# Performance work log

Hardware: AMD Instinct MI355X
Metric: run time of the kernel (lower is better)

## Reference

```python
import jax, jax.numpy as jnp
import numpy as np

CLASS_DIM = 4   # hardcoded in DsFunction1
PROTO_DIM = 20  # hardcoded in DsFunction1


def setup_inputs() -> dict:
    key = jax.random.key(0)
    k1, k2, k3 = jax.random.split(key, 3)
    B, C, H, Wd, D = 2, 16, 64, 64, 64
    inp = jax.random.normal(k1, (B, C, H, Wd, D), dtype=jnp.float32)
    W = jax.random.normal(k2, (PROTO_DIM, C), dtype=jnp.float32)
    BETA = jax.random.normal(k3, (PROTO_DIM, CLASS_DIM), dtype=jnp.float32) * 0.5
    alpha = jnp.zeros((PROTO_DIM, 1), dtype=jnp.float32)           # init 0 per reset_parameters
    gamma = jnp.full((PROTO_DIM, 1), 0.1, dtype=jnp.float32)       # init 0.1 per reset_parameters
    return {"input": inp, "W": W, "BETA": BETA, "alpha": alpha, "gamma": gamma}


def _ds_forward(x, W, BETA, alpha, gamma):
    # x: [B,C,H,Wd,D]; W: [K,C]; BETA: [K,M]; alpha, gamma: [K,1]
    B, C, H, Wd, D = x.shape
    BETA2 = BETA * BETA
    U = BETA2 / jnp.sum(BETA2, axis=1, keepdims=True)              # [K,M] membership weights
    alphap = 0.99 / (1.0 + jnp.exp(-alpha[:, 0]))                  # [K]

    # squared distances to prototypes: d[k] = 0.5 * ||x - W_k||^2 over channel dim
    x2 = jnp.sum(x * x, axis=1)                                    # [B,H,Wd,D]
    xw = jnp.einsum('bchwd,kc->kbhwd', x, W)                       # [K,B,H,Wd,D]
    w2 = jnp.sum(W * W, axis=1)                                    # [K]
    d = 0.5 * (x2[None] - 2.0 * xw + w2[:, None, None, None, None])  # [K,B,H,Wd,D]

    g2 = (gamma[:, 0] ** 2)[:, None, None, None, None]
    s = alphap[:, None, None, None, None] * jnp.exp(-g2 * d)       # [K,B,H,Wd,D]

    mfoc = U[:, :, None, None, None, None] * s[:, None]            # [K,M,B,H,Wd,D] focal masses
    momega = 1.0 - s                                               # [K,B,H,Wd,D] mass on Omega

    # sequential Dempster (unnormalized conjunctive) combination over prototypes
    def step(carry, km):
        mk_f, mk_o = carry                                         # [M,B,H,Wd,D], [B,H,Wd,D]
        m_f, m_o = km
        new_f = mk_f * (m_f + m_o[None]) + m_f * mk_o[None]
        new_o = mk_o * m_o
        return (new_f, new_o), None

    init = (jnp.zeros((CLASS_DIM, B, H, Wd, D), x.dtype),
            jnp.ones((B, H, Wd, D), x.dtype))
    (mk_f, mk_o), _ = jax.lax.scan(step, init, (mfoc, momega))

    mk = jnp.concatenate([mk_f, mk_o[None]], axis=0)               # [M+1,B,H,Wd,D]
    mk_n = mk / jnp.sum(mk, axis=0, keepdims=True)                 # normalize masses
    return jnp.transpose(mk_n, (1, 0, 2, 3, 4))                    # [B,M+1,H,Wd,D]


def reference(input, W, BETA, alpha, gamma):
    return _ds_forward(input, W, BETA, alpha, gamma)
```

## Files before the change

### kernel.cpp

```cpp
#include <hip/hip_runtime.h>
#include <hip/hip_bf16.h>
#include <math.h>

#define NK 20
#define NC 16
#define NM 4
#define TSTEP 2

typedef __attribute__((ext_vector_type(8)))  short  short8;
typedef __attribute__((ext_vector_type(16))) float  floatx16;

static __device__ __forceinline__ short bf16b(float f) {
    __hip_bfloat16 h = __float2bfloat16(f);
    return *reinterpret_cast<short*>(&h);
}

__global__ __launch_bounds__(256, 4) void ds_fused(
    const float* __restrict__ inp,
    const float* __restrict__ Wg,
    const float* __restrict__ BETAg,
    const float* __restrict__ alphag,
    const float* __restrict__ gammag,
    float* __restrict__ out,
    int S,
    int BS)
{
    __shared__ __align__(16) float sCst[32][8];
    __shared__ __align__(16) short sWpb[32][16];
    __shared__ short sA2[32][2];

    const int t = threadIdx.x;
    if (t < 32) {
        if (t < NK) {
            const float L   = 1.4426950408889634f;
            const float g   = gammag[t];
            const float g2L = g * g * L;
            float w2 = 0.f;
            #pragma unroll
            for (int c = 0; c < NC; ++c) {
                const float w = Wg[t*NC + c];
                sWpb[t][c] = bf16b(g2L * w);
                w2 = fmaf(w, w, w2);
            }
            const float a = 0.99f / (1.0f + __expf(-alphag[t]));
            float b0 = BETAg[t*NM+0], b1 = BETAg[t*NM+1], b2 = BETAg[t*NM+2], b3 = BETAg[t*NM+3];
            b0 *= b0; b1 *= b1; b2 *= b2; b3 *= b3;
            const float uinv = 1.0f / (b0 + b1 + b2 + b3);
            sCst[t][0] = (1.0f - b0*uinv) * a;
            sCst[t][1] = (1.0f - b1*uinv) * a;
            sCst[t][2] = (1.0f - b2*uinv) * a;
            sCst[t][3] = (1.0f - b3*uinv) * a;
            sCst[t][4] = a;
            sCst[t][5] = 0.f; sCst[t][6] = 0.f; sCst[t][7] = 0.f;
            sA2[t][0] = bf16b(-0.5f * g2L);
            sA2[t][1] = bf16b(-0.5f * g2L * w2);
        } else {
            #pragma unroll
            for (int i = 0; i < 8; ++i) sCst[t][i] = 0.f;
            #pragma unroll
            for (int c = 0; c < NC; ++c) sWpb[t][c] = 0;
            sA2[t][0] = 0; sA2[t][1] = 0;
        }
    }
    __syncthreads();

    const int lane = t & 63;
    const int half = lane >> 5;
    const int col  = lane & 31;
    const int gw   = blockIdx.x * 4 + (t >> 6);
    const int ebase = gw * (TSTEP * 32);

    const int b  = (ebase >= S) ? 1 : 0;
    const int spw = ebase - b * S;
    const float* xb0 = inp + (size_t)b * NC * S + spw + col;
    float xv[TSTEP][8];
    #pragma unroll
    for (int tt = 0; tt < TSTEP; ++tt)
        #pragma unroll
        for (int j = 0; j < 8; ++j)
            xv[tt][j] = xb0[(size_t)(8*half + j) * S + tt*32];

    const short8 afrag = *(const short8*)&sWpb[col][half*8];
    short8 a2frag;
    #pragma unroll
    for (int j = 0; j < 8; ++j) a2frag[j] = 0;
    if (half == 0) { a2frag[0] = sA2[col][0]; a2frag[1] = sA2[col][1]; }

    float cm0[12], cm1[12], cm2[12], cm3[12], cO[12];
    #pragma unroll
    for (int r = 0; r < 12; ++r) {
        const int p = (r & 3) + 8*(r >> 2) + 4*half;
        const float4 cv = *(const float4*)&sCst[p][0];
        cm0[r] = cv.x; cm1[r] = cv.y; cm2[r] = cv.z; cm3[r] = cv.w;
        cO[r]  = sCst[p][4];
    }

    #pragma unroll
    for (int tt = 0; tt < TSTEP; ++tt) {
        const int sp = spw + tt*32 + col;

        short8 bfrag;
        float x2p = 0.f;
        #pragma unroll
        for (int j = 0; j < 8; ++j) {
            const float v = xv[tt][j];
            x2p = fmaf(v, v, x2p);
            bfrag[j] = bf16b(v);
        }
        const float x2 = x2p + __shfl_xor(x2p, 32, 64);

        short8 b2frag;
        #pragma unroll
        for (int j = 0; j < 8; ++j) b2frag[j] = 0;
        if (half == 0) { b2frag[0] = bf16b(x2); b2frag[1] = (short)0x3F80; }

        floatx16 acc;
        #pragma unroll
        for (int i = 0; i < 16; ++i) acc[i] = 0.f;
        acc = __builtin_amdgcn_mfma_f32_32x32x16_bf16(afrag,  bfrag,  acc, 0, 0, 0);
        acc = __builtin_amdgcn_mfma_f32_32x32x16_bf16(a2frag, b2frag, acc, 0, 0, 0);

        float P0 = 1.f, P1 = 1.f, P2 = 1.f, P3 = 1.f, PO = 1.f;
        #pragma unroll
        for (int r = 0; r < 12; ++r) {
            const float ek = __builtin_amdgcn_exp2f(acc[r]);
            P0 *= fmaf(-cm0[r], ek, 1.0f);
            P1 *= fmaf(-cm1[r], ek, 1.0f);
            P2 *= fmaf(-cm2[r], ek, 1.0f);
            P3 *= fmaf(-cm3[r], ek, 1.0f);
            PO *= fmaf(-cO[r],  ek, 1.0f);
        }
        P0 *= __shfl_xor(P0, 32, 64);
        P1 *= __shfl_xor(P1, 32, 64);
        P2 *= __shfl_xor(P2, 32, 64);
        P3 *= __shfl_xor(P3, 32, 64);
        PO *= __shfl_xor(PO, 32, 64);

        const float O  = PO;
        const float f0 = P0 - O, f1 = P1 - O, f2 = P2 - O, f3 = P3 - O;
        const float inv = 1.0f / (f0 + f1 + f2 + f3 + O);

        float* op = out + (size_t)b * (NM+1) * S + sp;
        if (half == 0) {
            op[0]           = f0 * inv;
            op[(size_t)S]   = f1 * inv;
            op[(size_t)2*S] = f2 * inv;
        } else {
            op[(size_t)3*S] = f3 * inv;
            op[(size_t)4*S] = O  * inv;
        }
    }
}

extern "C" void kernel_launch(void* const* d_in, const int* in_sizes, int n_in,
                              void* d_out, int out_size, void* d_ws, size_t ws_size,
                              hipStream_t stream) {
    const float* inp   = (const float*)d_in[0];
    const float* Wg    = (const float*)d_in[1];
    const float* BETAg = (const float*)d_in[2];
    const float* alphag= (const float*)d_in[3];
    const float* gammag= (const float*)d_in[4];
    float* out = (float*)d_out;

    const int BS = in_sizes[0] / NC;
    const int S  = BS / 2;

    const int elems_per_block = 4 * TSTEP * 32;
    const int grid = (BS + elems_per_block - 1) / elems_per_block;
    ds_fused<<<grid, 256, 0, stream>>>(inp, Wg, BETAg, alphag, gammag, out, S, BS);
}
```

Before: 85.61 us.

## Stage input through LDS with float4 loads and double per-wave work

Each wave now covers 128 spatial elements instead of 64. It loads its input as 16-byte float4 vectors, issued before the constant setup so the global latency overlaps that work. The data is then transposed through a padded per-wave LDS buffer into the MFMA B-fragment layout. This cuts the number of global load instructions and halves the grid, at the cost of about 33KB of LDS per block, which may limit occupancy under the 4-block launch bound. The grid computation drops the ceiling division and now assumes BS is divisible by 512.

Result: slower. 102.1 us (+19.3%).

```diff
diff --git a/kernel.cpp b/kernel.cpp
--- a/kernel.cpp
+++ b/kernel.cpp
@@ -5,7 +5,7 @@
 #define NK 20
 #define NC 16
 #define NM 4
-#define TSTEP 2
+#define LDSW 132
 
 typedef __attribute__((ext_vector_type(8)))  short  short8;
 typedef __attribute__((ext_vector_type(16))) float  floatx16;
@@ -28,8 +28,26 @@
     __shared__ __align__(16) float sCst[32][8];
     __shared__ __align__(16) short sWpb[32][16];
     __shared__ short sA2[32][2];
+    __shared__ __align__(16) float sX[4][NC][LDSW];
 
-    const int t = threadIdx.x;
+    const int t    = threadIdx.x;
+    const int lane = t & 63;
+    const int half = lane >> 5;
+    const int col  = lane & 31;
+    const int w    = t >> 6;
+
+    const int ebase = (blockIdx.x * 4 + w) * 128;
+    const int b     = (ebase >= S) ? 1 : 0;
+    const int spw   = ebase - b * S;
+    const float* xb = inp + (size_t)b * NC * S + spw;
+
+    float4 xv[8];
+    #pragma unroll
+    for (int cc = 0; cc < 8; ++cc) {
+        const int ch = 2*cc + half;
+        xv[cc] = *(const float4*)(xb + (size_t)ch * S + 4*col);
+    }
+
     if (t < 32) {
         if (t < NK) {
             const float L   = 1.4426950408889634f;
@@ -38,9 +56,9 @@
             float w2 = 0.f;
             #pragma unroll
             for (int c = 0; c < NC; ++c) {
-                const float w = Wg[t*NC + c];
-                sWpb[t][c] = bf16b(g2L * w);
-                w2 = fmaf(w, w, w2);
+                const float wv = Wg[t*NC + c];
+                sWpb[t][c] = bf16b(g2L * wv);
+                w2 = fmaf(wv, wv, w2);
             }
             const float a = 0.99f / (1.0f + __expf(-alphag[t]));
             float b0 = BETAg[t*NM+0], b1 = BETAg[t*NM+1], b2 = BETAg[t*NM+2], b3 = BETAg[t*NM+3];
@@ -64,21 +82,11 @@
     }
     __syncthreads();
 
-    const int lane = t & 63;
-    const int half = lane >> 5;
-    const int col  = lane & 31;
-    const int gw   = blockIdx.x * 4 + (t >> 6);
-    const int ebase = gw * (TSTEP * 32);
-
-    const int b  = (ebase >= S) ? 1 : 0;
-    const int spw = ebase - b * S;
-    const float* xb0 = inp + (size_t)b * NC * S + spw + col;
-    float xv[TSTEP][8];
     #pragma unroll
-    for (int tt = 0; tt < TSTEP; ++tt)
-        #pragma unroll
-        for (int j = 0; j < 8; ++j)
-            xv[tt][j] = xb0[(size_t)(8*half + j) * S + tt*32];
+    for (int cc = 0; cc < 8; ++cc) {
+        const int ch = 2*cc + half;
+        *(float4*)&sX[w][ch][4*col] = xv[cc];
+    }
 
     const short8 afrag = *(const short8*)&sWpb[col][half*8];
     short8 a2frag;
@@ -95,15 +103,15 @@
         cO[r]  = sCst[p][4];
     }
 
+    float* ob = out + (size_t)b * (NM+1) * S + spw;
+
     #pragma unroll
-    for (int tt = 0; tt < TSTEP; ++tt) {
-        const int sp = spw + tt*32 + col;
-
+    for (int tt = 0; tt < 4; ++tt) {
         short8 bfrag;
         float x2p = 0.f;
         #pragma unroll
         for (int j = 0; j < 8; ++j) {
-            const float v = xv[tt][j];
+            const float v = sX[w][8*half + j][tt*32 + col];
             x2p = fmaf(v, v, x2p);
             bfrag[j] = bf16b(v);
         }
@@ -140,7 +148,7 @@
         const float f0 = P0 - O, f1 = P1 - O, f2 = P2 - O, f3 = P3 - O;
         const float inv = 1.0f / (f0 + f1 + f2 + f3 + O);
 
-        float* op = out + (size_t)b * (NM+1) * S + sp;
+        float* op = ob + tt*32 + col;
         if (half == 0) {
             op[0]           = f0 * inv;
             op[(size_t)S]   = f1 * inv;
@@ -165,7 +173,6 @@
     const int BS = in_sizes[0] / NC;
     const int S  = BS / 2;
 
-    const int elems_per_block = 4 * TSTEP * 32;
-    const int grid = (BS + elems_per_block - 1) / elems_per_block;
+    const int grid = BS / 512;
     ds_fused<<<grid, 256, 0, stream>>>(inp, Wg, BETAg, alphag, gammag, out, S, BS);
 }
```

## Issue input loads before constant setup and process four tiles per wave

Applied to the files above, without the earlier changes.

The per-wave global loads of the input channels now start before the shared-memory constant setup and the barrier, so load latency overlaps the prototype preprocessing. Each wave now handles four 32-element tiles instead of two, which halves the grid and amortises the setup over more work. The Omega coefficient is rebuilt in registers from the four class coefficients, since they sum to three times alpha, dropping one shared load per row. The launch grid is hard-coded to BS/512, which drops remainder handling, and the smaller grid lowers occupancy.

New measurement: 87.43 us. +2.1%, slower.

```diff
diff --git a/kernel.cpp b/kernel.cpp
--- a/kernel.cpp
+++ b/kernel.cpp
@@ -5,7 +5,7 @@
 #define NK 20
 #define NC 16
 #define NM 4
-#define TSTEP 2
+#define TSTEP 4
 
 typedef __attribute__((ext_vector_type(8)))  short  short8;
 typedef __attribute__((ext_vector_type(16))) float  floatx16;
@@ -29,7 +29,23 @@
     __shared__ __align__(16) short sWpb[32][16];
     __shared__ short sA2[32][2];
 
-    const int t = threadIdx.x;
+    const int t    = threadIdx.x;
+    const int lane = t & 63;
+    const int half = lane >> 5;
+    const int col  = lane & 31;
+
+    const int ebase = (blockIdx.x * 4 + (t >> 6)) * (TSTEP * 32);
+    const int b     = (ebase >= S) ? 1 : 0;
+    const int spw   = ebase - b * S;
+    const float* xb = inp + (size_t)b * NC * S + spw + col;
+
+    float xv[TSTEP][8];
+    #pragma unroll
+    for (int tt = 0; tt < TSTEP; ++tt)
+        #pragma unroll
+        for (int j = 0; j < 8; ++j)
+            xv[tt][j] = xb[(size_t)(8*half + j) * S + tt*32];
+
     if (t < 32) {
         if (t < NK) {
             const float L   = 1.4426950408889634f;
@@ -38,9 +54,9 @@
             float w2 = 0.f;
             #pragma unroll
             for (int c = 0; c < NC; ++c) {
-                const float w = Wg[t*NC + c];
-                sWpb[t][c] = bf16b(g2L * w);
-                w2 = fmaf(w, w, w2);
+                const float wv = Wg[t*NC + c];
+                sWpb[t][c] = bf16b(g2L * wv);
+                w2 = fmaf(wv, wv, w2);
             }
             const float a = 0.99f / (1.0f + __expf(-alphag[t]));
             float b0 = BETAg[t*NM+0], b1 = BETAg[t*NM+1], b2 = BETAg[t*NM+2], b3 = BETAg[t*NM+3];
@@ -64,41 +80,28 @@
     }
     __syncthreads();
 
-    const int lane = t & 63;
-    const int half = lane >> 5;
-    const int col  = lane & 31;
-    const int gw   = blockIdx.x * 4 + (t >> 6);
-    const int ebase = gw * (TSTEP * 32);
-
-    const int b  = (ebase >= S) ? 1 : 0;
-    const int spw = ebase - b * S;
-    const float* xb0 = inp + (size_t)b * NC * S + spw + col;
-    float xv[TSTEP][8];
-    #pragma unroll
-    for (int tt = 0; tt < TSTEP; ++tt)
-        #pragma unroll
-        for (int j = 0; j < 8; ++j)
-            xv[tt][j] = xb0[(size_t)(8*half + j) * S + tt*32];
-
     const short8 afrag = *(const short8*)&sWpb[col][half*8];
     short8 a2frag;
     #pragma unroll
     for (int j = 0; j < 8; ++j) a2frag[j] = 0;
     if (half == 0) { a2frag[0] = sA2[col][0]; a2frag[1] = sA2[col][1]; }
 
-    float cm0[12], cm1[12], cm2[12], cm3[12], cO[12];
+    float4 cm[12];
     #pragma unroll
     for (int r = 0; r < 12; ++r) {
         const int p = (r & 3) + 8*(r >> 2) + 4*half;
-        const float4 cv = *(const float4*)&sCst[p][0];
-        cm0[r] = cv.x; cm1[r] = cv.y; cm2[r] = cv.z; cm3[r] = cv.w;
-        cO[r]  = sCst[p][4];
+        cm[r] = *(const float4*)&sCst[p][0];
     }
+
+    short8 b2base;
+    #pragma unroll
+    for (int j = 0; j < 8; ++j) b2base[j] = 0;
+    if (half == 0) b2base[1] = (short)0x3F80;
+
+    float* ob = out + (size_t)b * (NM+1) * S + spw + col;
 
     #pragma unroll
     for (int tt = 0; tt < TSTEP; ++tt) {
-        const int sp = spw + tt*32 + col;
-
         short8 bfrag;
         float x2p = 0.f;
         #pragma unroll
@@ -109,10 +112,8 @@
         }
         const float x2 = x2p + __shfl_xor(x2p, 32, 64);
 
-        short8 b2frag;
-        #pragma unroll
-        for (int j = 0; j < 8; ++j) b2frag[j] = 0;
-        if (half == 0) { b2frag[0] = bf16b(x2); b2frag[1] = (short)0x3F80; }
+        short8 b2frag = b2base;
+        if (half == 0) b2frag[0] = bf16b(x2);
 
         floatx16 acc;
         #pragma unroll
@@ -124,11 +125,12 @@
         #pragma unroll
         for (int r = 0; r < 12; ++r) {
             const float ek = __builtin_amdgcn_exp2f(acc[r]);
-            P0 *= fmaf(-cm0[r], ek, 1.0f);
-            P1 *= fmaf(-cm1[r], ek, 1.0f);
-            P2 *= fmaf(-cm2[r], ek, 1.0f);
-            P3 *= fmaf(-cm3[r], ek, 1.0f);
-            PO *= fmaf(-cO[r],  ek, 1.0f);
+            const float cO = (cm[r].x + cm[r].y + cm[r].z + cm[r].w) * (1.0f/3.0f);
+            P0 *= fmaf(-cm[r].x, ek, 1.0f);
+            P1 *= fmaf(-cm[r].y, ek, 1.0f);
+            P2 *= fmaf(-cm[r].z, ek, 1.0f);
+            P3 *= fmaf(-cm[r].w, ek, 1.0f);
+            PO *= fmaf(-cO,      ek, 1.0f);
         }
         P0 *= __shfl_xor(P0, 32, 64);
         P1 *= __shfl_xor(P1, 32, 64);
@@ -140,7 +142,7 @@
         const float f0 = P0 - O, f1 = P1 - O, f2 = P2 - O, f3 = P3 - O;
         const float inv = 1.0f / (f0 + f1 + f2 + f3 + O);
 
-        float* op = out + (size_t)b * (NM+1) * S + sp;
+        float* op = ob + tt*32;
         if (half == 0) {
             op[0]           = f0 * inv;
             op[(size_t)S]   = f1 * inv;
@@ -165,7 +167,6 @@
     const int BS = in_sizes[0] / NC;
     const int S  = BS / 2;
 
-    const int elems_per_block = 4 * TSTEP * 32;
-    const int grid = (BS + elems_per_block - 1) / elems_per_block;
+    const int grid = BS / 512;
     ds_fused<<<grid, 256, 0, stream>>>(inp, Wg, BETAg, alphag, gammag, out, S, BS);
 }
```
